# Kernel optimization log

Hardware: AMD Instinct MI355X
Metric: run time of the kernel (lower is better)

The kernel has to match this reference:

```python
import jax, jax.numpy as jnp
import numpy as np

EPS = 1e-6  # NAFNet LayerNorm2d eps
C = 64
B, H, W = 4, 128, 512


def _layer_norm_c(x, w, b):
    # x: [B,H,W,C]; normalize over channel dim (LayerNorm2d semantics)
    mu = jnp.mean(x, axis=-1, keepdims=True)
    var = jnp.mean(jnp.square(x - mu), axis=-1, keepdims=True)
    return (x - mu) * jax.lax.rsqrt(var + EPS) * w + b


def setup_inputs() -> dict:
    key = jax.random.key(0)
    ks = jax.random.split(key, 8)
    std = 1.0 / np.sqrt(C)  # conv1x1 fan-in init scale
    return {
        "x_l": jax.random.normal(ks[0], (B, C, H, W), jnp.float32),
        "x_r": jax.random.normal(ks[1], (B, C, H, W), jnp.float32),
        "norm_l_w": jnp.ones((C,), jnp.float32),
        "norm_l_b": jnp.zeros((C,), jnp.float32),
        "norm_r_w": jnp.ones((C,), jnp.float32),
        "norm_r_b": jnp.zeros((C,), jnp.float32),
        "l1_w": jax.random.normal(ks[2], (C, C), jnp.float32) * std,
        "l1_b": jnp.zeros((C,), jnp.float32),
        "r1_w": jax.random.normal(ks[3], (C, C), jnp.float32) * std,
        "r1_b": jnp.zeros((C,), jnp.float32),
        "l2_w": jax.random.normal(ks[4], (C, C), jnp.float32) * std,
        "l2_b": jnp.zeros((C,), jnp.float32),
        "r2_w": jax.random.normal(ks[5], (C, C), jnp.float32) * std,
        "r2_b": jnp.zeros((C,), jnp.float32),
        "beta": jax.random.normal(ks[6], (C,), jnp.float32) * 0.1,
        "gamma": jax.random.normal(ks[7], (C,), jnp.float32) * 0.1,
    }


def reference(x_l, x_r, norm_l_w, norm_l_b, norm_r_w, norm_r_b,
              l1_w, l1_b, r1_w, r1_b, l2_w, l2_b, r2_w, r2_b, beta, gamma):
    c = x_l.shape[1]
    scale = c ** (-0.5)
    # NCHW -> NHWC for channel-last math
    xl = jnp.transpose(x_l, (0, 2, 3, 1))  # [B,H,W,C]
    xr = jnp.transpose(x_r, (0, 2, 3, 1))

    # 1x1 conv == per-pixel linear: y = x @ W^T + b (W is [out,in])
    Q_l = jnp.einsum("bhwc,oc->bhwo", _layer_norm_c(xl, norm_l_w, norm_l_b), l1_w) + l1_b
    Q_r = jnp.einsum("bhwc,oc->bhwo", _layer_norm_c(xr, norm_r_w, norm_r_b), r1_w) + r1_b
    V_l = jnp.einsum("bhwc,oc->bhwo", xl, l2_w) + l2_b
    V_r = jnp.einsum("bhwc,oc->bhwo", xr, r2_w) + r2_b

    # row-wise cross-attention scores: [B,H,W_l,W_r]
    att = jnp.einsum("bhwc,bhvc->bhwv", Q_l, Q_r) * scale

    # right->left: softmax over W_r (last axis)
    F_r2l = jnp.einsum("bhwv,bhvc->bhwc", jax.nn.softmax(att, axis=-1), V_r)
    # left->right: softmax over W_l (axis -2 of att)
    F_l2r = jnp.einsum("bhwv,bhwc->bhvc", jax.nn.softmax(att, axis=-2), V_l)

    out_l = x_l + jnp.transpose(F_r2l * beta, (0, 3, 1, 2))
    out_r = x_r + jnp.transpose(F_l2r * gamma, (0, 3, 1, 2))
    return out_l, out_r
```

## Files before the change

kernel.cpp:

```cpp
#include <hip/hip_runtime.h>
#include <hip/hip_bf16.h>

#define HW_   65536
#define CHW_  4194304
#define OUTR_ 16777216
#define QSZ_  16777216

typedef __attribute__((ext_vector_type(4))) float    f32x4;
typedef __attribute__((ext_vector_type(8))) short    s16x8;
typedef __attribute__((ext_vector_type(4))) short    s16x4;
typedef __attribute__((ext_vector_type(4))) unsigned u32x4;
typedef __attribute__((ext_vector_type(2))) unsigned u32x2;

#define MFMA32(A,B,C) __builtin_amdgcn_mfma_f32_16x16x32_bf16((A),(B),(C),0,0,0)

#if __has_builtin(__builtin_amdgcn_mfma_f32_16x16x16bf16_1k)
#define MFMA16(A,B,C) __builtin_amdgcn_mfma_f32_16x16x16bf16_1k((A),(B),(C),0,0,0)
#else
__device__ __forceinline__ f32x4 mfma16_asm(s16x4 a, s16x4 b, f32x4 c){
  asm volatile("v_mfma_f32_16x16x16_bf16 %0, %1, %2, %0\n\ts_nop 7" : "+v"(c) : "v"(a), "v"(b));
  return c;
}
#define MFMA16(A,B,C) mfma16_asm((A),(B),(C))
#endif

#if __has_builtin(__builtin_amdgcn_exp2f)
#define EXP2(x) __builtin_amdgcn_exp2f(x)
#else
__device__ __forceinline__ float exp2_hw(float x){
  float r; asm("v_exp_f32 %0, %1\n\ts_nop 0" : "=v"(r) : "v"(x)); return r;
}
#define EXP2(x) exp2_hw(x)
#endif

#define QSCALE  0.18033688011112043f
#define SQSCALE 0.42466090350f

__device__ __forceinline__ unsigned short bf16u(float f) {
  union { __hip_bfloat16 h; unsigned short s; } x; x.h = __float2bfloat16(f); return x.s;
}
__device__ __forceinline__ unsigned pack2(float a, float b) {
  return (unsigned)bf16u(a) | ((unsigned)bf16u(b) << 16);
}
__device__ __forceinline__ float bflo(unsigned u) {
  union { unsigned q; float f; } x; x.q = u << 16; return x.f;
}
__device__ __forceinline__ float bfhi(unsigned u) {
  union { unsigned q; float f; } x; x.q = u & 0xFFFF0000u; return x.f;
}
__device__ __forceinline__ s16x8 as_s16x8(u32x4 u){ union{u32x4 a; s16x8 b;} x; x.a=u; return x.b; }
__device__ __forceinline__ s16x4 as_s16x4(u32x2 u){ union{u32x2 a; s16x4 b;} x; x.a=u; return x.b; }

__device__ __forceinline__ int swz128(int row, int bir) { return row*128 + (bir ^ ((row&7)<<4)); }
__device__ __forceinline__ int swzV(int c, int bir)    { return c*1024 + (bir ^ ((c&63)<<4)); }

__device__ __forceinline__ void ln32(const float* __restrict__ p, int base, int pix, int half,
                                     const float* __restrict__ w, const float* __restrict__ bb,
                                     char* buf, float* redS, float* redSS) {
  const int c0 = half*32;
  float xv[32], s = 0.f, ss = 0.f;
#pragma unroll
  for (int i = 0; i < 32; ++i) {
    float v = p[base + (c0+i)*HW_ + pix];
    xv[i] = v; s += v; ss = fmaf(v, v, ss);
  }
  redS[half*512 + pix] = s; redSS[half*512 + pix] = ss;
  __syncthreads();
  float st  = redS[pix]  + redS[512 + pix];
  float sst = redSS[pix] + redSS[512 + pix];
  float mu = st * 0.015625f;
  float rs = rsqrtf(fmaxf(sst * 0.015625f - mu*mu, 0.f) + 1e-6f);
#pragma unroll
  for (int i2 = 0; i2 < 4; ++i2) {
    u32x4 u;
#pragma unroll
    for (int e = 0; e < 4; ++e) {
      int i = i2*8 + e*2;
      float y0 = (xv[i  ]-mu)*rs*w[c0+i  ] + bb[c0+i  ];
      float y1 = (xv[i+1]-mu)*rs*w[c0+i+1] + bb[c0+i+1];
      u[e] = pack2(y0, y1);
    }
    *(u32x4*)(buf + swz128(pix, half*64 + i2*16)) = u;
  }
}

__device__ __forceinline__ void stageW(const float* __restrict__ Wg, char* bufW, int t) {
  int row = t >> 3, c0 = (t & 7) * 8;
  f32x4 f0 = *(const f32x4*)(Wg + row*64 + c0);
  f32x4 f1 = *(const f32x4*)(Wg + row*64 + c0 + 4);
  u32x4 u = { pack2(f0[0],f0[1]), pack2(f0[2],f0[3]), pack2(f1[0],f1[1]), pack2(f1[2],f1[3]) };
  *(u32x4*)(bufW + swz128(row, c0*2)) = u;
}

__device__ __forceinline__ void epi32(const char* bufG, const float* __restrict__ xres,
                                      const float* __restrict__ coef, float* __restrict__ outp,
                                      int base, int pix, int half) {
  const int c0 = half*32;
#pragma unroll
  for (int i2 = 0; i2 < 4; ++i2) {
    u32x4 gv = *(const u32x4*)(bufG + swz128(pix, half*64 + i2*16));
#pragma unroll
    for (int e = 0; e < 4; ++e) {
      int i = i2*8 + e*2;
      int idx = base + (c0+i)*HW_ + pix;
      outp[idx]       = xres[idx]       + coef[c0+i]   * bflo(gv[e]);
      outp[idx + HW_] = xres[idx + HW_] + coef[c0+i+1] * bfhi(gv[e]);
    }
  }
}

__global__ __launch_bounds__(1024)
void k1_prep(const float* __restrict__ xl, const float* __restrict__ xr,
             const float* __restrict__ nlw, const float* __restrict__ nlb,
             const float* __restrict__ nrw, const float* __restrict__ nrb,
             const float* __restrict__ l1w, const float* __restrict__ l1b,
             const float* __restrict__ r1w, const float* __restrict__ r1b,
             unsigned short* __restrict__ Qws) {
  __shared__ __align__(16) char bufA[65536];
  __shared__ __align__(16) char bufW[8192];
  __shared__ float redS[1024], redSS[1024];
  const int t = threadIdx.x, lane = t & 63, wave = t >> 6;
  const int pix = t & 511, half = t >> 9;
  const int g = lane >> 4, q15 = lane & 15;
  const int bh = blockIdx.x, b = bh >> 7, h = bh & 127;
  const int base = b*CHW_ + h*512;

#pragma unroll 1
  for (int s = 0; s < 2; ++s) {
    const float* x  = s ? xr  : xl;
    const float* w  = s ? nrw : nlw;
    const float* bb = s ? nrb : nlb;
    const float* W  = s ? r1w : l1w;
    const float* bi = s ? r1b : l1b;
    unsigned short* Qd = Qws + s*QSZ_ + bh*32768;
    if (s) __syncthreads();
    ln32(x, base, pix, half, w, bb, bufA, redS, redSS);
    if (t < 512) stageW(W, bufW, t);
    __syncthreads();
    {
      u32x4 a[2][2], wb[4][2];
#pragma unroll
      for (int mt = 0; mt < 2; ++mt)
#pragma unroll
        for (int hh = 0; hh < 2; ++hh)
          a[mt][hh] = *(const u32x4*)(bufA + swz128(wave*32 + mt*16 + q15, hh*64 + g*16));
#pragma unroll
      for (int ot = 0; ot < 4; ++ot)
#pragma unroll
        for (int hh = 0; hh < 2; ++hh)
          wb[ot][hh] = *(const u32x4*)(bufW + swz128(ot*16 + q15, hh*64 + g*16));
#pragma unroll
      for (int mt = 0; mt < 2; ++mt)
#pragma unroll
        for (int ot = 0; ot < 4; ++ot) {
          f32x4 z = {0.f,0.f,0.f,0.f};
          f32x4 acc = MFMA32(as_s16x8(a[mt][0]), as_s16x8(wb[ot][0]), z);
          acc = MFMA32(as_s16x8(a[mt][1]), as_s16x8(wb[ot][1]), acc);
          float bv = bi[ot*16 + q15];
#pragma unroll
          for (int rr = 0; rr < 4; ++rr)
            *(short*)(bufA + swz128(wave*32 + mt*16 + 4*g + rr, 2*(ot*16 + q15))) =
                (short)bf16u((acc[rr] + bv) * SQSCALE);
        }
    }
    __syncthreads();
#pragma unroll
    for (int i = 0; i < 4; ++i) {
      int seg = t*4 + i, row = seg >> 3, b16 = (seg & 7) * 16;
      u32x4 v = *(const u32x4*)(bufA + swz128(row, b16));
      *(u32x4*)((char*)Qd + row*128 + b16) = v;
    }
  }
}

__global__ __launch_bounds__(512)
void k2_flash(const unsigned short* __restrict__ Qws,
              const float* __restrict__ xl, const float* __restrict__ xr,
              unsigned short* __restrict__ Ows) {
  __shared__ __align__(16) char Kc[2][8192];
  __shared__ __align__(16) char Vc[2][8192];
  const int t = threadIdx.x, lane = t & 63, wave = t >> 6;
  const int g = lane >> 4, q15 = lane & 15;
  const int bid = blockIdx.x, qh = bid & 1, dir = (bid >> 1) & 1, bh = bid >> 2;
  const int b = bh >> 7, h = bh & 127;
  const int base = b*CHW_ + h*512;
  const char* Qb = (const char*)(Qws + dir*QSZ_ + bh*32768);
  const char* Kb = (const char*)(Qws + (1-dir)*QSZ_ + bh*32768);
  const float* xV = dir ? xl : xr;
  unsigned short* Ob = Ows + (2+dir)*QSZ_ + bh*32768;

  const int qrow0 = qh*256 + wave*32;
  s16x8 qf[2][2];
#pragma unroll
  for (int qt = 0; qt < 2; ++qt)
#pragma unroll
    for (int hh = 0; hh < 2; ++hh)
      qf[qt][hh] = as_s16x8(*(const u32x4*)(Qb + (qrow0 + qt*16 + q15)*128 + hh*64 + g*16));

  const int srow = t >> 3, sg = (t & 7) * 16, kv0 = (t & 7) * 8;
  {
    *(u32x4*)(Kc[0] + swz128(srow, sg)) = *(const u32x4*)(Kb + srow*128 + sg);
    f32x4 f0 = *(const f32x4*)(xV + base + srow*HW_ + kv0);
    f32x4 f1 = *(const f32x4*)(xV + base + srow*HW_ + kv0 + 4);
    u32x4 vv = { pack2(f0[0],f0[1]), pack2(f0[2],f0[3]), pack2(f1[0],f1[1]), pack2(f1[2],f1[3]) };
    *(u32x4*)(Vc[0] + swz128(srow, sg)) = vv;
  }
  __syncthreads();

  float lsum[2] = {0.f, 0.f};
  f32x4 O[2][4];
#pragma unroll
  for (int qt = 0; qt < 2; ++qt)
#pragma unroll
    for (int ct = 0; ct < 4; ++ct) { f32x4 z = {0.f,0.f,0.f,0.f}; O[qt][ct] = z; }

#pragma unroll 1
  for (int ch = 0; ch < 8; ++ch) {
    const int cur = ch & 1;
    u32x4 kreg; f32x4 nf0, nf1;
    if (ch < 7) {
      kreg = *(const u32x4*)(Kb + ((ch+1)*64 + srow)*128 + sg);
      nf0  = *(const f32x4*)(xV + base + srow*HW_ + (ch+1)*64 + kv0);
      nf1  = *(const f32x4*)(xV + base + srow*HW_ + (ch+1)*64 + kv0 + 4);
    }
#pragma unroll
    for (int qt = 0; qt < 2; ++qt) {
      u32x2 pa[4];
      float sml = 0.f;
#pragma unroll
      for (int kb = 0; kb < 4; ++kb) {
        u32x4 k0 = *(const u32x4*)(Kc[cur] + swz128(kb*16 + q15, g*16));
        u32x4 k1 = *(const u32x4*)(Kc[cur] + swz128(kb*16 + q15, 64 + g*16));
        f32x4 z = {0.f,0.f,0.f,0.f};
        f32x4 s = MFMA32(as_s16x8(k0), qf[qt][0], z);
        s = MFMA32(as_s16x8(k1), qf[qt][1], s);
        float p0 = EXP2(s[0]), p1 = EXP2(s[1]), p2 = EXP2(s[2]), p3 = EXP2(s[3]);
        sml += (p0 + p1) + (p2 + p3);
        u32x2 pp = { pack2(p0, p1), pack2(p2, p3) };
        pa[kb] = pp;
      }
      lsum[qt] += sml;
#pragma unroll
      for (int ct = 0; ct < 4; ++ct) {
        int c = ct*16 + q15;
#pragma unroll
        for (int kb = 0; kb < 4; ++kb) {
          u32x2 vb = *(const u32x2*)(Vc[cur] + swz128(c, kb*32 + 8*g));
          O[qt][ct] = MFMA16(as_s16x4(pa[kb]), as_s16x4(vb), O[qt][ct]);
        }
      }
    }
    if (ch < 7) {
      *(u32x4*)(Kc[cur^1] + swz128(srow, sg)) = kreg;
      u32x4 vv = { pack2(nf0[0],nf0[1]), pack2(nf0[2],nf0[3]), pack2(nf1[0],nf1[1]), pack2(nf1[2],nf1[3]) };
      *(u32x4*)(Vc[cur^1] + swz128(srow, sg)) = vv;
    }
    __syncthreads();
  }
#pragma unroll
  for (int qt = 0; qt < 2; ++qt) {
    float l = lsum[qt];
    l += __shfl_xor(l, 16);
    l += __shfl_xor(l, 32);
    float inv = 1.f / l;
    float invr[4];
#pragma unroll
    for (int rr = 0; rr < 4; ++rr) invr[rr] = __shfl(inv, 4*g + rr);
#pragma unroll
    for (int ct = 0; ct < 4; ++ct)
#pragma unroll
      for (int rr = 0; rr < 4; ++rr)
        Ob[(qrow0 + qt*16 + 4*g + rr)*64 + ct*16 + q15] =
            (unsigned short)bf16u(O[qt][ct][rr] * invr[rr]);
  }
}

__global__ __launch_bounds__(1024)
void k3_epi(const unsigned short* __restrict__ Qws,
            const float* __restrict__ xl, const float* __restrict__ xr,
            const float* __restrict__ l2w, const float* __restrict__ l2b,
            const float* __restrict__ r2w, const float* __restrict__ r2b,
            const float* __restrict__ beta, const float* __restrict__ gamma,
            float* __restrict__ out) {
  __shared__ __align__(16) char bufG[65536];
  __shared__ __align__(16) char bufW[8192];
  const int t = threadIdx.x, lane = t & 63, wave = t >> 6;
  const int g = lane >> 4, q15 = lane & 15;
  const int pix = t & 511, half = t >> 9;
  const int bid = blockIdx.x, dir = bid & 1, bh = bid >> 1;
  const int b = bh >> 7, h = bh & 127;
  const int base = b*CHW_ + h*512;
  const float* W    = dir ? l2w : r2w;
  const float* bi   = dir ? l2b : r2b;
  const float* cf   = dir ? gamma : beta;
  const float* xres = dir ? xr  : xl;
  float* outp = out + dir*OUTR_;
  const char* Ob = (const char*)(Qws + (2+dir)*QSZ_ + bh*32768);

  if (t < 512) stageW(W, bufW, t);
  __syncthreads();
  {
    u32x4 a[2][2], wb[4][2];
#pragma unroll
    for (int mt = 0; mt < 2; ++mt)
#pragma unroll
      for (int hh = 0; hh < 2; ++hh)
        a[mt][hh] = *(const u32x4*)(Ob + (wave*32 + mt*16 + q15)*128 + hh*64 + g*16);
#pragma unroll
    for (int ot = 0; ot < 4; ++ot)
#pragma unroll
      for (int hh = 0; hh < 2; ++hh)
        wb[ot][hh] = *(const u32x4*)(bufW + swz128(ot*16 + q15, hh*64 + g*16));
#pragma unroll
    for (int mt = 0; mt < 2; ++mt)
#pragma unroll
      for (int ot = 0; ot < 4; ++ot) {
        f32x4 z = {0.f,0.f,0.f,0.f};
        f32x4 acc = MFMA32(as_s16x8(a[mt][0]), as_s16x8(wb[ot][0]), z);
        acc = MFMA32(as_s16x8(a[mt][1]), as_s16x8(wb[ot][1]), acc);
        float bv = bi[ot*16 + q15];
#pragma unroll
        for (int rr = 0; rr < 4; ++rr)
          *(short*)(bufG + swz128(wave*32 + mt*16 + 4*g + rr, 2*(ot*16 + q15))) =
              (short)bf16u(acc[rr] + bv);
      }
  }
  __syncthreads();
  epi32(bufG, xres, cf, outp, base, pix, half);
}

__device__ __forceinline__ void stageV_m(const float* __restrict__ x, int base, char* bufV, int t) {
  int c = t >> 4, w0 = (t & 15) * 32;
#pragma unroll
  for (int i = 0; i < 4; ++i) {
    int w = w0 + i*8;
    f32x4 f0 = *(const f32x4*)(x + base + c*HW_ + w);
    f32x4 f1 = *(const f32x4*)(x + base + c*HW_ + w + 4);
    u32x4 u = { pack2(f0[0],f0[1]), pack2(f0[2],f0[3]), pack2(f1[0],f1[1]), pack2(f1[2],f1[3]) };
    *(u32x4*)(bufV + swzV(c, w*2)) = u;
  }
}
__device__ __forceinline__ void proj64_m(const char* bufIn, const char* bufW,
                                         const float* __restrict__ biasG,
                                         char* bufOut, int wave, int lane) {
  int g = lane >> 4, q15 = lane & 15;
  u32x4 a[2][2], wb[4][2];
#pragma unroll
  for (int mt = 0; mt < 2; ++mt)
#pragma unroll
    for (int h = 0; h < 2; ++h)
      a[mt][h] = *(const u32x4*)(bufIn + swz128(wave*32 + mt*16 + q15, h*64 + g*16));
#pragma unroll
  for (int ot = 0; ot < 4; ++ot)
#pragma unroll
    for (int h = 0; h < 2; ++h)
      wb[ot][h] = *(const u32x4*)(bufW + swz128(ot*16 + q15, h*64 + g*16));
#pragma unroll
  for (int mt = 0; mt < 2; ++mt)
#pragma unroll
    for (int ot = 0; ot < 4; ++ot) {
      f32x4 z = {0.f,0.f,0.f,0.f};
      f32x4 acc = MFMA32(as_s16x8(a[mt][0]), as_s16x8(wb[ot][0]), z);
      acc = MFMA32(as_s16x8(a[mt][1]), as_s16x8(wb[ot][1]), acc);
      float bv = biasG[ot*16 + q15];
#pragma unroll
      for (int rr = 0; rr < 4; ++rr)
        *(short*)(bufOut + swz128(wave*32 + mt*16 + 4*g + rr, 2*(ot*16 + q15))) =
            (short)bf16u(acc[rr] + bv);
    }
}
__device__ __forceinline__ void extract_q_m(const char* bufQ, int wave, int lane, s16x8 (&qf)[2][2]) {
  int g = lane >> 4, q15 = lane & 15;
#pragma unroll
  for (int qt = 0; qt < 2; ++qt)
#pragma unroll
    for (int h = 0; h < 2; ++h) {
      u32x4 u = *(const u32x4*)(bufQ + swz128(wave*32 + qt*16 + q15, h*64 + g*16));
#pragma unroll
      for (int e = 0; e < 4; ++e)
        u[e] = pack2(bflo(u[e])*QSCALE, bfhi(u[e])*QSCALE);
      qf[qt][h] = as_s16x8(u);
    }
}
__device__ __forceinline__ void flash_m(const char* bufK, const char* bufV, const s16x8 (&qf)[2][2],
                                        f32x4 (&O)[2][4], float (&lsum)[2], int lane) {
  int g = lane >> 4, q15 = lane & 15;
  float mref[2];
#pragma unroll
  for (int qt = 0; qt < 2; ++qt) {
    mref[qt] = -__builtin_inff(); lsum[qt] = 0.f;
#pragma unroll
    for (int ct = 0; ct < 4; ++ct) { f32x4 z = {0.f,0.f,0.f,0.f}; O[qt][ct] = z; }
  }
#pragma unroll 1
  for (int ch = 0; ch < 16; ++ch) {
    int kbase = ch * 32;
    u32x4 ka[2][2];
#pragma unroll
    for (int kb = 0; kb < 2; ++kb)
#pragma unroll
      for (int h = 0; h < 2; ++h)
        ka[kb][h] = *(const u32x4*)(bufK + swz128(kbase + kb*16 + q15, h*64 + g*16));
#pragma unroll
    for (int qt = 0; qt < 2; ++qt) {
      f32x4 z = {0.f,0.f,0.f,0.f};
      f32x4 a0 = MFMA32(as_s16x8(ka[0][0]), qf[qt][0], z);
      a0 = MFMA32(as_s16x8(ka[0][1]), qf[qt][1], a0);
      f32x4 a1 = MFMA32(as_s16x8(ka[1][0]), qf[qt][0], z);
      a1 = MFMA32(as_s16x8(ka[1][1]), qf[qt][1], a1);
      float cm = fmaxf(fmaxf(fmaxf(a0[0],a0[1]), fmaxf(a0[2],a0[3])),
                       fmaxf(fmaxf(a1[0],a1[1]), fmaxf(a1[2],a1[3])));
      cm = fmaxf(cm, __shfl_xor(cm, 16));
      cm = fmaxf(cm, __shfl_xor(cm, 32));
      if (__any(cm > mref[qt] + 8.f)) {
        float nm = fmaxf(mref[qt], cm);
        float corr = EXP2(mref[qt] - nm);
        lsum[qt] *= corr; mref[qt] = nm;
#pragma unroll
        for (int rr = 0; rr < 4; ++rr) {
          float cr = __shfl(corr, 4*g + rr);
#pragma unroll
          for (int ct = 0; ct < 4; ++ct) O[qt][ct][rr] *= cr;
        }
      }
      float p[8], sm = 0.f;
#pragma unroll
      for (int j = 0; j < 4; ++j) { p[j]   = EXP2(a0[j] - mref[qt]); sm += p[j]; }
#pragma unroll
      for (int j = 0; j < 4; ++j) { p[4+j] = EXP2(a1[j] - mref[qt]); sm += p[4+j]; }
      float s1 = sm + __shfl_xor(sm, 16);
      lsum[qt] += s1 + __shfl_xor(s1, 32);
      u32x2 pa0 = { pack2(p[0],p[1]), pack2(p[2],p[3]) };
      u32x2 pa1 = { pack2(p[4],p[5]), pack2(p[6],p[7]) };
#pragma unroll
      for (int ct = 0; ct < 4; ++ct) {
        int c = ct*16 + q15;
        u32x2 v0 = *(const u32x2*)(bufV + swzV(c, (kbase + 4*g)*2));
        u32x2 v1 = *(const u32x2*)(bufV + swzV(c, (kbase + 16 + 4*g)*2));
        O[qt][ct] = MFMA16(as_s16x4(pa0), as_s16x4(v0), O[qt][ct]);
        O[qt][ct] = MFMA16(as_s16x4(pa1), as_s16x4(v1), O[qt][ct]);
      }
    }
  }
}
__device__ __forceinline__ void write_O_m(char* buf, const f32x4 (&O)[2][4], const float (&lsum)[2],
                                          int wave, int lane) {
  int g = lane >> 4, q15 = lane & 15;
#pragma unroll
  for (int qt = 0; qt < 2; ++qt) {
    float inv = 1.f / lsum[qt];
    float invr[4];
#pragma unroll
    for (int rr = 0; rr < 4; ++rr) invr[rr] = __shfl(inv, 4*g + rr);
#pragma unroll
    for (int ct = 0; ct < 4; ++ct)
#pragma unroll
      for (int rr = 0; rr < 4; ++rr)
        *(short*)(buf + swz128(wave*32 + qt*16 + 4*g + rr, 2*(ct*16 + q15))) =
            (short)bf16u(O[qt][ct][rr] * invr[rr]);
  }
}
__device__ __forceinline__ void epi_ln_m(const char* bufG, const float* __restrict__ xres,
                                         const float* __restrict__ coef, float* __restrict__ outp,
                                         const float* __restrict__ w, const float* __restrict__ bb,
                                         char* bufLN, int base, int pix, int half,
                                         float* redS, float* redSS) {
  const int c0 = half*32;
  float xv[32], s = 0.f, ss = 0.f;
#pragma unroll
  for (int i2 = 0; i2 < 4; ++i2) {
    u32x4 gv = *(const u32x4*)(bufG + swz128(pix, half*64 + i2*16));
#pragma unroll
    for (int e = 0; e < 4; ++e) {
      int i = i2*8 + e*2;
      int idx = base + (c0+i)*HW_ + pix;
      float x0 = xres[idx], x1 = xres[idx + HW_];
      xv[i] = x0; xv[i+1] = x1;
      s += x0 + x1; ss = fmaf(x0,x0,ss); ss = fmaf(x1,x1,ss);
      outp[idx]       = x0 + coef[c0+i]   * bflo(gv[e]);
      outp[idx + HW_] = x1 + coef[c0+i+1] * bfhi(gv[e]);
    }
  }
  redS[half*512 + pix] = s; redSS[half*512 + pix] = ss;
  __syncthreads();
  float st  = redS[pix]  + redS[512 + pix];
  float sst = redSS[pix] + redSS[512 + pix];
  float mu = st * 0.015625f;
  float rs = rsqrtf(fmaxf(sst * 0.015625f - mu*mu, 0.f) + 1e-6f);
#pragma unroll
  for (int i2 = 0; i2 < 4; ++i2) {
    u32x4 u;
#pragma unroll
    for (int e = 0; e < 4; ++e) {
      int i = i2*8 + e*2;
      float y0 = (xv[i  ]-mu)*rs*w[c0+i  ] + bb[c0+i  ];
      float y1 = (xv[i+1]-mu)*rs*w[c0+i+1] + bb[c0+i+1];
      u[e] = pack2(y0, y1);
    }
    *(u32x4*)(bufLN + swz128(pix, half*64 + i2*16)) = u;
  }
}

__global__ __launch_bounds__(1024)
void scam_mono(const float* __restrict__ xl, const float* __restrict__ xr,
               const float* __restrict__ nlw, const float* __restrict__ nlb,
               const float* __restrict__ nrw, const float* __restrict__ nrb,
               const float* __restrict__ l1w, const float* __restrict__ l1b,
               const float* __restrict__ r1w, const float* __restrict__ r1b,
               const float* __restrict__ l2w, const float* __restrict__ l2b,
               const float* __restrict__ r2w, const float* __restrict__ r2b,
               const float* __restrict__ beta, const float* __restrict__ gamma,
               float* __restrict__ out) {
  __shared__ __align__(16) char bufA[65536];
  __shared__ __align__(16) char bufB[65536];
  __shared__ __align__(16) char bufW[8192];
  __shared__ float redS[1024];
  __shared__ float redSS[1024];
  const int t = threadIdx.x, lane = t & 63, wave = t >> 6;
  const int pix = t & 511, half = t >> 9;
  const int r = blockIdx.x, b = r >> 7, h = r & 127;
  const int base = b*CHW_ + h*512;

  if (t < 512) stageW(l1w, bufW, t);
  ln32(xl, base, pix, half, nlw, nlb, bufA, redS, redSS);
  __syncthreads();
  proj64_m(bufA, bufW, l1b, bufB, wave, lane);
  __syncthreads();
  s16x8 qfL[2][2];
  extract_q_m(bufB, wave, lane, qfL);
  if (t < 512) stageW(r1w, bufW, t);
  ln32(xr, base, pix, half, nrw, nrb, bufA, redS, redSS);
  __syncthreads();
  proj64_m(bufA, bufW, r1b, bufB, wave, lane);
  __syncthreads();
  stageV_m(xr, base, bufA, t);
  if (t < 512) stageW(r2w, bufW, t);
  __syncthreads();
  f32x4 O[2][4]; float lsum[2];
  flash_m(bufB, bufA, qfL, O, lsum, lane);
  s16x8 qfR[2][2];
  extract_q_m(bufB, wave, lane, qfR);
  __syncthreads();
  write_O_m(bufA, O, lsum, wave, lane);
  __syncthreads();
  proj64_m(bufA, bufW, r2b, bufB, wave, lane);
  __syncthreads();
  if (t < 512) stageW(l1w, bufW, t);
  epi_ln_m(bufB, xl, beta, out, nlw, nlb, bufA, base, pix, half, redS, redSS);
  __syncthreads();
  proj64_m(bufA, bufW, l1b, bufB, wave, lane);
  __syncthreads();
  stageV_m(xl, base, bufA, t);
  if (t < 512) stageW(l2w, bufW, t);
  __syncthreads();
  flash_m(bufB, bufA, qfR, O, lsum, lane);
  __syncthreads();
  write_O_m(bufA, O, lsum, wave, lane);
  __syncthreads();
  proj64_m(bufA, bufW, l2b, bufB, wave, lane);
  __syncthreads();
  epi32(bufB, xr, gamma, out + OUTR_, base, pix, half);
}

extern "C" void kernel_launch(void* const* d_in, const int* in_sizes, int n_in,
                              void* d_out, int out_size, void* d_ws, size_t ws_size,
                              hipStream_t stream) {
  (void)in_sizes; (void)n_in; (void)out_size;
  const float* xl  = (const float*)d_in[0];
  const float* xr  = (const float*)d_in[1];
  const float* nlw = (const float*)d_in[2];
  const float* nlb = (const float*)d_in[3];
  const float* nrw = (const float*)d_in[4];
  const float* nrb = (const float*)d_in[5];
  const float* l1w = (const float*)d_in[6];
  const float* l1b = (const float*)d_in[7];
  const float* r1w = (const float*)d_in[8];
  const float* r1b = (const float*)d_in[9];
  const float* l2w = (const float*)d_in[10];
  const float* l2b = (const float*)d_in[11];
  const float* r2w = (const float*)d_in[12];
  const float* r2b = (const float*)d_in[13];
  const float* beta  = (const float*)d_in[14];
  const float* gamma = (const float*)d_in[15];
  float* out = (float*)d_out;

  if (ws_size >= (size_t)4 * QSZ_ * sizeof(unsigned short)) {
    unsigned short* Qws = (unsigned short*)d_ws;
    k1_prep<<<dim3(512), dim3(1024), 0, stream>>>(
        xl, xr, nlw, nlb, nrw, nrb, l1w, l1b, r1w, r1b, Qws);
    k2_flash<<<dim3(2048), dim3(512), 0, stream>>>(Qws, xl, xr, Qws);
    k3_epi<<<dim3(1024), dim3(1024), 0, stream>>>(
        Qws, xl, xr, l2w, l2b, r2w, r2b, beta, gamma, out);
  } else {
    scam_mono<<<dim3(512), dim3(1024), 0, stream>>>(
        xl, xr, nlw, nlb, nrw, nrb, l1w, l1b, r1w, r1b,
        l2w, l2b, r2w, r2b, beta, gamma, out);
  }
}
```

Baseline: 221.7 us.

## Fuse attention and output projection epilogue into one kernel

Merges the flash-attention kernel with the epilogue kernel, so the unnormalized attention output stays in LDS. The 1x1 V-projection (exploiting linearity to apply the softmax normalization and bias after projection) and the residual write happen in the same block. This removes a bf16 workspace round trip and one kernel launch, and halves the workspace requirement. The cost is a larger LDS footprint per block, extra syncs, and narrower per-block epilogue stores over 256 pixels.

```diff
diff --git a/kernel.cpp b/kernel.cpp
--- a/kernel.cpp
+++ b/kernel.cpp
@@ -174,11 +174,18 @@
 }
 
 __global__ __launch_bounds__(512)
-void k2_flash(const unsigned short* __restrict__ Qws,
+void k2_fused(const unsigned short* __restrict__ Qws,
               const float* __restrict__ xl, const float* __restrict__ xr,
-              unsigned short* __restrict__ Ows) {
-  __shared__ __align__(16) char Kc[2][8192];
-  __shared__ __align__(16) char Vc[2][8192];
+              const float* __restrict__ l2w, const float* __restrict__ l2b,
+              const float* __restrict__ r2w, const float* __restrict__ r2b,
+              const float* __restrict__ beta, const float* __restrict__ gamma,
+              float* __restrict__ out) {
+  __shared__ __align__(16) char ldsM[40960];
+  __shared__ float lsumS[256];
+  char* const Kc0 = ldsM;
+  char* const Vc0 = ldsM + 16384;
+  char* const bufW = ldsM + 32768;
+
   const int t = threadIdx.x, lane = t & 63, wave = t >> 6;
   const int g = lane >> 4, q15 = lane & 15;
   const int bid = blockIdx.x, qh = bid & 1, dir = (bid >> 1) & 1, bh = bid >> 2;
@@ -186,8 +193,12 @@
   const int base = b*CHW_ + h*512;
   const char* Qb = (const char*)(Qws + dir*QSZ_ + bh*32768);
   const char* Kb = (const char*)(Qws + (1-dir)*QSZ_ + bh*32768);
-  const float* xV = dir ? xl : xr;
-  unsigned short* Ob = Ows + (2+dir)*QSZ_ + bh*32768;
+  const float* xV   = dir ? xl : xr;
+  const float* xres = dir ? xr : xl;
+  const float* W2   = dir ? l2w : r2w;
+  const float* b2   = dir ? l2b : r2b;
+  const float* cf   = dir ? gamma : beta;
+  float* outp = out + dir*OUTR_;
 
   const int qrow0 = qh*256 + wave*32;
   s16x8 qf[2][2];
@@ -197,13 +208,15 @@
     for (int hh = 0; hh < 2; ++hh)
       qf[qt][hh] = as_s16x8(*(const u32x4*)(Qb + (qrow0 + qt*16 + q15)*128 + hh*64 + g*16));
 
+  stageW(W2, bufW, t);
+
   const int srow = t >> 3, sg = (t & 7) * 16, kv0 = (t & 7) * 8;
   {
-    *(u32x4*)(Kc[0] + swz128(srow, sg)) = *(const u32x4*)(Kb + srow*128 + sg);
+    *(u32x4*)(Kc0 + swz128(srow, sg)) = *(const u32x4*)(Kb + srow*128 + sg);
     f32x4 f0 = *(const f32x4*)(xV + base + srow*HW_ + kv0);
     f32x4 f1 = *(const f32x4*)(xV + base + srow*HW_ + kv0 + 4);
     u32x4 vv = { pack2(f0[0],f0[1]), pack2(f0[2],f0[3]), pack2(f1[0],f1[1]), pack2(f1[2],f1[3]) };
-    *(u32x4*)(Vc[0] + swz128(srow, sg)) = vv;
+    *(u32x4*)(Vc0 + swz128(srow, sg)) = vv;
   }
   __syncthreads();
 
@@ -216,7 +229,8 @@
 
 #pragma unroll 1
   for (int ch = 0; ch < 8; ++ch) {
-    const int cur = ch & 1;
+    char* const Kc = Kc0 + (ch & 1)*8192;
+    char* const Vc = Vc0 + (ch & 1)*8192;
     u32x4 kreg; f32x4 nf0, nf1;
     if (ch < 7) {
       kreg = *(const u32x4*)(Kb + ((ch+1)*64 + srow)*128 + sg);
@@ -229,8 +243,8 @@
       float sml = 0.f;
 #pragma unroll
       for (int kb = 0; kb < 4; ++kb) {
-        u32x4 k0 = *(const u32x4*)(Kc[cur] + swz128(kb*16 + q15, g*16));
-        u32x4 k1 = *(const u32x4*)(Kc[cur] + swz128(kb*16 + q15, 64 + g*16));
+        u32x4 k0 = *(const u32x4*)(Kc + swz128(kb*16 + q15, g*16));
+        u32x4 k1 = *(const u32x4*)(Kc + swz128(kb*16 + q15, 64 + g*16));
         f32x4 z = {0.f,0.f,0.f,0.f};
         f32x4 s = MFMA32(as_s16x8(k0), qf[qt][0], z);
         s = MFMA32(as_s16x8(k1), qf[qt][1], s);
@@ -245,67 +259,43 @@
         int c = ct*16 + q15;
 #pragma unroll
         for (int kb = 0; kb < 4; ++kb) {
-          u32x2 vb = *(const u32x2*)(Vc[cur] + swz128(c, kb*32 + 8*g));
+          u32x2 vb = *(const u32x2*)(Vc + swz128(c, kb*32 + 8*g));
           O[qt][ct] = MFMA16(as_s16x4(pa[kb]), as_s16x4(vb), O[qt][ct]);
         }
       }
     }
     if (ch < 7) {
-      *(u32x4*)(Kc[cur^1] + swz128(srow, sg)) = kreg;
+      char* const Kn = Kc0 + ((ch & 1)^1)*8192;
+      char* const Vn = Vc0 + ((ch & 1)^1)*8192;
+      *(u32x4*)(Kn + swz128(srow, sg)) = kreg;
       u32x4 vv = { pack2(nf0[0],nf0[1]), pack2(nf0[2],nf0[3]), pack2(nf1[0],nf1[1]), pack2(nf1[2],nf1[3]) };
-      *(u32x4*)(Vc[cur^1] + swz128(srow, sg)) = vv;
+      *(u32x4*)(Vn + swz128(srow, sg)) = vv;
     }
     __syncthreads();
   }
+
 #pragma unroll
   for (int qt = 0; qt < 2; ++qt) {
     float l = lsum[qt];
     l += __shfl_xor(l, 16);
     l += __shfl_xor(l, 32);
-    float inv = 1.f / l;
-    float invr[4];
-#pragma unroll
-    for (int rr = 0; rr < 4; ++rr) invr[rr] = __shfl(inv, 4*g + rr);
+    if (lane < 16) lsumS[wave*32 + qt*16 + q15] = l;
 #pragma unroll
     for (int ct = 0; ct < 4; ++ct)
 #pragma unroll
       for (int rr = 0; rr < 4; ++rr)
-        Ob[(qrow0 + qt*16 + 4*g + rr)*64 + ct*16 + q15] =
-            (unsigned short)bf16u(O[qt][ct][rr] * invr[rr]);
-  }
-}
-
-__global__ __launch_bounds__(1024)
-void k3_epi(const unsigned short* __restrict__ Qws,
-            const float* __restrict__ xl, const float* __restrict__ xr,
-            const float* __restrict__ l2w, const float* __restrict__ l2b,
-            const float* __restrict__ r2w, const float* __restrict__ r2b,
-            const float* __restrict__ beta, const float* __restrict__ gamma,
-            float* __restrict__ out) {
-  __shared__ __align__(16) char bufG[65536];
-  __shared__ __align__(16) char bufW[8192];
-  const int t = threadIdx.x, lane = t & 63, wave = t >> 6;
-  const int g = lane >> 4, q15 = lane & 15;
-  const int pix = t & 511, half = t >> 9;
-  const int bid = blockIdx.x, dir = bid & 1, bh = bid >> 1;
-  const int b = bh >> 7, h = bh & 127;
-  const int base = b*CHW_ + h*512;
-  const float* W    = dir ? l2w : r2w;
-  const float* bi   = dir ? l2b : r2b;
-  const float* cf   = dir ? gamma : beta;
-  const float* xres = dir ? xr  : xl;
-  float* outp = out + dir*OUTR_;
-  const char* Ob = (const char*)(Qws + (2+dir)*QSZ_ + bh*32768);
-
-  if (t < 512) stageW(W, bufW, t);
-  __syncthreads();
+        *(short*)(ldsM + swz128(wave*32 + qt*16 + 4*g + rr, 2*(ct*16 + q15))) =
+            (short)bf16u(O[qt][ct][rr]);
+  }
+  __syncthreads();
+
   {
     u32x4 a[2][2], wb[4][2];
 #pragma unroll
     for (int mt = 0; mt < 2; ++mt)
 #pragma unroll
       for (int hh = 0; hh < 2; ++hh)
-        a[mt][hh] = *(const u32x4*)(Ob + (wave*32 + mt*16 + q15)*128 + hh*64 + g*16);
+        a[mt][hh] = *(const u32x4*)(ldsM + swz128(wave*32 + mt*16 + q15, hh*64 + g*16));
 #pragma unroll
     for (int ot = 0; ot < 4; ++ot)
 #pragma unroll
@@ -318,15 +308,31 @@
         f32x4 z = {0.f,0.f,0.f,0.f};
         f32x4 acc = MFMA32(as_s16x8(a[mt][0]), as_s16x8(wb[ot][0]), z);
         acc = MFMA32(as_s16x8(a[mt][1]), as_s16x8(wb[ot][1]), acc);
-        float bv = bi[ot*16 + q15];
 #pragma unroll
         for (int rr = 0; rr < 4; ++rr)
-          *(short*)(bufG + swz128(wave*32 + mt*16 + 4*g + rr, 2*(ot*16 + q15))) =
-              (short)bf16u(acc[rr] + bv);
+          *(short*)(ldsM + swz128(wave*32 + mt*16 + 4*g + rr, 2*(ot*16 + q15))) =
+              (short)bf16u(acc[rr]);
       }
   }
   __syncthreads();
-  epi32(bufG, xres, cf, outp, base, pix, half);
+
+  {
+    const int pl = t & 255, half2 = t >> 8;
+    const int pix = qh*256 + pl;
+    const float il = 1.f / lsumS[pl];
+    const int c0 = half2*32;
+#pragma unroll
+    for (int i2 = 0; i2 < 4; ++i2) {
+      u32x4 gv = *(const u32x4*)(ldsM + swz128(pl, half2*64 + i2*16));
+#pragma unroll
+      for (int e = 0; e < 4; ++e) {
+        int c = c0 + i2*8 + e*2;
+        int idx = base + c*HW_ + pix;
+        outp[idx]       = xres[idx]       + cf[c]  *(bflo(gv[e])*il + b2[c]);
+        outp[idx + HW_] = xres[idx + HW_] + cf[c+1]*(bfhi(gv[e])*il + b2[c+1]);
+      }
+    }
+  }
 }
 
 __device__ __forceinline__ void stageV_m(const float* __restrict__ x, int base, char* bufV, int t) {
@@ -584,12 +590,11 @@
   const float* gamma = (const float*)d_in[15];
   float* out = (float*)d_out;
 
-  if (ws_size >= (size_t)4 * QSZ_ * sizeof(unsigned short)) {
+  if (ws_size >= (size_t)2 * QSZ_ * sizeof(unsigned short)) {
     unsigned short* Qws = (unsigned short*)d_ws;
     k1_prep<<<dim3(512), dim3(1024), 0, stream>>>(
         xl, xr, nlw, nlb, nrw, nrb, l1w, l1b, r1w, r1b, Qws);
-    k2_flash<<<dim3(2048), dim3(512), 0, stream>>>(Qws, xl, xr, Qws);
-    k3_epi<<<dim3(1024), dim3(1024), 0, stream>>>(
+    k2_fused<<<dim3(2048), dim3(512), 0, stream>>>(
         Qws, xl, xr, l2w, l2b, r2w, r2b, beta, gamma, out);
   } else {
     scam_mono<<<dim3(512), dim3(1024), 0, stream>>>(
```

Measured after the change: 190.0 us. 1.17x faster.
